# Kernel tuning notes

Hardware: AMD Instinct MI355X
Metric: run time of the kernel (lower is better)

Reference implementation:

```python
import jax, jax.numpy as jnp
import numpy as np

D_MODEL = 512
D_INNER = 1024   # expand * d_model
NH = 16          # heads (headdim 64)
HD = 64
NS = 16          # d_state
HID = 1024       # ff hidden = expand * d_model


def _ln(x, w, b, eps=1e-5):
    m = x.mean(-1, keepdims=True)
    v = ((x - m) ** 2).mean(-1, keepdims=True)
    return (x - m) * jax.lax.rsqrt(v + eps) * w + b


def _rms(x, w, eps=1e-5):
    return x * jax.lax.rsqrt((x * x).mean(-1, keepdims=True) + eps) * w


def _tree_scan(dt, xh, Bv, Cv, pidx, A):
    # dt:[B,T,W,H] xh:[B,T,W,H,P] Bv,Cv:[B,T,W,N] pidx:[B,T,W] A:[H]
    B_, T, W, H = dt.shape
    P = xh.shape[-1]
    N = Bv.shape[-1]
    h0 = jnp.zeros((B_, W, H, P, N), dt.dtype)
    xs = (jnp.moveaxis(dt, 1, 0), jnp.moveaxis(xh, 1, 0),
          jnp.moveaxis(Bv, 1, 0), jnp.moveaxis(Cv, 1, 0),
          jnp.moveaxis(pidx, 1, 0))

    def step(h, inp):
        dt_t, xh_t, b_t, c_t, p_t = inp
        # gather parent state from previous level along the width axis
        hp = jnp.take_along_axis(h, p_t[:, :, None, None, None], axis=1)  # [B,W,H,P,N]
        dA = jnp.exp(dt_t * A)                                            # [B,W,H]
        h_new = dA[..., None, None] * hp \
              + dt_t[..., None, None] * xh_t[..., None] * b_t[:, :, None, None, :]
        y_t = jnp.einsum('bwhpn,bwn->bwhp', h_new, c_t)
        return h_new, y_t

    _, ys = jax.lax.scan(step, h0, xs)
    return jnp.moveaxis(ys, 0, 1)  # [B,T,W,H,P]


def setup_inputs() -> dict:
    key = jax.random.key(0)
    ks = jax.random.split(key, 12)
    B, T, W = 8, 64, 16
    d_in_proj = 2 * D_INNER + 2 * NS + NH  # z | x | B | C | dt
    inp = {
        'x': jax.random.normal(ks[0], (B, T, W, D_MODEL), jnp.float32),
        'parent_pos': jax.random.randint(ks[1], (B, T, W), 0, W, dtype=jnp.int32),
        'ln1_w': jnp.ones((D_MODEL,), jnp.float32),
        'ln1_b': jnp.zeros((D_MODEL,), jnp.float32),
        'in_w': jax.random.normal(ks[2], (D_MODEL, d_in_proj), jnp.float32) * 0.02,
        'in_b': jnp.zeros((d_in_proj,), jnp.float32),
        'A_log': jnp.log(jax.random.uniform(ks[3], (NH,), jnp.float32, 1.0, 16.0)),
        'dt_bias': jnp.full((NH,), -4.0, jnp.float32),
        'Dp': jnp.ones((NH,), jnp.float32),
        'norm_w': jnp.ones((D_INNER,), jnp.float32),
        'out_w': jax.random.normal(ks[4], (D_INNER, D_MODEL), jnp.float32) * 0.02,
        'out_b': jnp.zeros((D_MODEL,), jnp.float32),
        'ln2_w': jnp.ones((D_MODEL,), jnp.float32),
        'ln2_b': jnp.zeros((D_MODEL,), jnp.float32),
        'ff1_w': jax.random.normal(ks[5], (D_MODEL, 2 * HID), jnp.float32) * 0.02,
        'ff1_b': jnp.zeros((2 * HID,), jnp.float32),
        'ff2_w': jax.random.normal(ks[6], (HID, D_MODEL), jnp.float32) * 0.02,
        'ff2_b': jnp.zeros((D_MODEL,), jnp.float32),
    }
    return inp


def reference(x, parent_pos, ln1_w, ln1_b, in_w, in_b, A_log, dt_bias, Dp,
              norm_w, out_w, out_b, ln2_w, ln2_b, ff1_w, ff1_b, ff2_w, ff2_b):
    # norm1 + TreeMamba2 + residual
    xn = _ln(x, ln1_w, ln1_b)
    proj = xn @ in_w + in_b
    z, xp, Bv, Cv, dtr = jnp.split(
        proj, [D_INNER, 2 * D_INNER, 2 * D_INNER + NS, 2 * D_INNER + 2 * NS], axis=-1)
    dt = jax.nn.softplus(dtr + dt_bias)            # [B,T,W,NH]
    A = -jnp.exp(A_log)                            # [NH]
    xh = xp.reshape(*xp.shape[:-1], NH, HD)        # [B,T,W,NH,HD]
    y = _tree_scan(dt, xh, Bv, Cv, parent_pos, A)  # [B,T,W,NH,HD]
    y = y + Dp[..., None] * xh                     # skip connection D*x
    y = y.reshape(*y.shape[:-2], D_INNER)
    y = _rms(y * jax.nn.silu(z), norm_w)           # gated RMSNorm
    y = y @ out_w + out_b
    x = y + x
    # norm2 + gated FF + residual
    yn = _ln(x, ln2_w, ln2_b)
    f = yn @ ff1_w + ff1_b
    f1, g = jnp.split(f, 2, axis=-1)
    f = (f1 * jax.nn.silu(g)) @ ff2_w + ff2_b
    return x + f
```

## Files before the change

### kernel.cpp

```cpp
#include <hip/hip_runtime.h>
#include <hip/hip_bf16.h>
#include <cmath>

#define D_MODEL 512
#define D_INNER 1024
#define NHEAD 16
#define HDIM 64
#define NSTATE 16
#define NB 8
#define NT 64
#define NW 16
#define MROWS 8192
#define NPROJ 2096

typedef __attribute__((ext_vector_type(8))) short short8;
typedef __attribute__((ext_vector_type(4))) float f32x4;
typedef __hip_bfloat16 bf16;
typedef unsigned int u32;
typedef unsigned short u16;

__device__ __forceinline__ u32 fbits(float f) { return __float_as_uint(f); }
__device__ __forceinline__ float ubits(u32 u) { return __uint_as_float(u); }
__device__ __forceinline__ u32 pack_bf(float a, float b) {
  return (fbits(b) & 0xffff0000u) | (fbits(a) >> 16);
}

template<int N> __device__ __forceinline__ void vmwait() {
  if constexpr (N == 0)      asm volatile("s_waitcnt vmcnt(0)" ::: "memory");
  else if constexpr (N == 2) asm volatile("s_waitcnt vmcnt(2)" ::: "memory");
  else if constexpr (N == 3) asm volatile("s_waitcnt vmcnt(3)" ::: "memory");
  else if constexpr (N == 4) asm volatile("s_waitcnt vmcnt(4)" ::: "memory");
  else if constexpr (N == 6) asm volatile("s_waitcnt vmcnt(6)" ::: "memory");
  else if constexpr (N == 8) asm volatile("s_waitcnt vmcnt(8)" ::: "memory");
  else static_assert(N == 0, "unsupported vmcnt");
}

__device__ __forceinline__ float block_sum(float v, float* sbuf) {
#pragma unroll
  for (int o = 32; o > 0; o >>= 1) v += __shfl_down(v, o, 64);
  int lane = threadIdx.x & 63, wid = threadIdx.x >> 6;
  if (lane == 0) sbuf[wid] = v;
  __syncthreads();
  if (threadIdx.x == 0) {
    float t = 0.f;
    for (int i = 0; i < 4; i++) t += sbuf[i];
    sbuf[0] = t;
  }
  __syncthreads();
  return sbuf[0];
}

__global__ __launch_bounds__(256) void ln512_bf16_kernel(
    const float* __restrict__ x, const float* __restrict__ w,
    const float* __restrict__ b, bf16* __restrict__ out) {
  __shared__ float s1[8], s2[8];
  int row = blockIdx.x;
  const float* xr = x + (size_t)row * D_MODEL;
  bf16* outr = out + (size_t)row * D_MODEL;
  int c0 = threadIdx.x, c1 = threadIdx.x + 256;
  float v0 = xr[c0], v1 = xr[c1];
  float s  = block_sum(v0 + v1, s1);
  float ss = block_sum(v0 * v0 + v1 * v1, s2);
  float mean = s * (1.f / 512.f);
  float var  = ss * (1.f / 512.f) - mean * mean;
  float inv  = rsqrtf(var + 1e-5f);
  outr[c0] = __float2bfloat16((v0 - mean) * inv * w[c0] + b[c0]);
  outr[c1] = __float2bfloat16((v1 - mean) * inv * w[c1] + b[c1]);
}

__global__ __launch_bounds__(256) void wconv_all_kernel(
    const float* __restrict__ in_w, bf16* __restrict__ in_wt,
    const float* __restrict__ out_w, bf16* __restrict__ out_wt,
    const float* __restrict__ ff1_w, bf16* __restrict__ ff1_wt,
    const float* __restrict__ ff2_w, bf16* __restrict__ ff2_wt) {
  __shared__ float tile[32][33];
  int id = blockIdx.x;
  const float* w; bf16* wt;
  int K, N, Npad, bx, by;
  if (id < 1088)      { w = in_w;  wt = in_wt;  K = 512;  N = NPROJ; Npad = 2176; bx = id % 68;  by = id / 68; }
  else if (id < 1600) { int j = id - 1088; w = out_w; wt = out_wt; K = 1024; N = 512;  Npad = 512;  bx = j % 16; by = j / 16; }
  else if (id < 2624) { int j = id - 1600; w = ff1_w; wt = ff1_wt; K = 512;  N = 2048; Npad = 2048; bx = j % 64; by = j / 64; }
  else                { int j = id - 2624; w = ff2_w; wt = ff2_wt; K = 1024; N = 512;  Npad = 512;  bx = j % 16; by = j / 16; }
  int n0 = bx * 32, k0 = by * 32;
  int tx = threadIdx.x & 31, ty = threadIdx.x >> 5;
#pragma unroll
  for (int i = 0; i < 4; i++) {
    int k = k0 + ty + i * 8, n = n0 + tx;
    tile[ty + i * 8][tx] = (k < K && n < N) ? w[(size_t)k * N + n] : 0.f;
  }
  __syncthreads();
#pragma unroll
  for (int i = 0; i < 4; i++) {
    int n = n0 + ty + i * 8, k = k0 + tx;
    if (n < Npad && k < K)
      wt[(size_t)n * K + k] = __float2bfloat16(tile[tx][ty + i * 8]);
  }
}

template<int BM, int BN, int WN, int MR, int NR>
__global__ __launch_bounds__(256) void mfma_gemm_kernel(
    const bf16* __restrict__ A, const bf16* __restrict__ Bt,
    const float* __restrict__ bias, int nbias,
    const float* __restrict__ resid,
    float* __restrict__ C, int ldc, int K) {
  constexpr int ROWS = BM + BN;
  constexpr int ISS  = ROWS / 64;
  __shared__ __align__(16) bf16 sAB[3][ROWS][32];

  int wid = threadIdx.x >> 6, lane = threadIdx.x & 63;
  int row0 = blockIdx.y * BM, col0 = blockIdx.x * BN;
  int wr = (wid / WN) * (MR * 16);
  int wc = (wid % WN) * (NR * 16);
  int lr = lane >> 2;
  int lc = (lane & 3) * 8;

  f32x4 acc[MR][NR];
#pragma unroll
  for (int m = 0; m < MR; m++)
#pragma unroll
    for (int n = 0; n < NR; n++) acc[m][n] = (f32x4){0.f, 0.f, 0.f, 0.f};

  auto stage = [&](int buf, int k0) {
#pragma unroll
    for (int i = 0; i < ISS; i++) {
      int rb = (wid * ISS + i) * 16;
      int r = rb + lr;
      const bf16* src = (r < BM)
          ? A  + (size_t)(row0 + r) * K + k0 + lc
          : Bt + (size_t)(col0 + (r - BM)) * K + k0 + lc;
      __builtin_amdgcn_global_load_lds(
          (const __attribute__((address_space(1))) void*)src,
          (__attribute__((address_space(3))) void*)&sAB[buf][rb][0], 16, 0, 0);
    }
  };

  stage(0, 0);
  stage(1, 32);
  int cur = 0;
  for (int k0 = 0; k0 < K; k0 += 32) {
    if (k0 + 32 < K) vmwait<ISS>(); else vmwait<0>();
    __builtin_amdgcn_s_barrier();
    asm volatile("" ::: "memory");
    if (k0 + 64 < K) stage(cur == 0 ? 2 : cur - 1, k0 + 64);
    short8 a[MR], b[NR];
    int kk = (lane >> 4) * 8;
#pragma unroll
    for (int m = 0; m < MR; m++)
      a[m] = *(const short8*)&sAB[cur][wr + m * 16 + (lane & 15)][kk];
#pragma unroll
    for (int n = 0; n < NR; n++)
      b[n] = *(const short8*)&sAB[cur][BM + wc + n * 16 + (lane & 15)][kk];
#pragma unroll
    for (int m = 0; m < MR; m++)
#pragma unroll
      for (int n = 0; n < NR; n++)
        acc[m][n] = __builtin_amdgcn_mfma_f32_16x16x32_bf16(a[m], b[n], acc[m][n], 0, 0, 0);
    asm volatile("" ::: "memory");
    cur = (cur == 2) ? 0 : cur + 1;
  }

  int crow = row0 + wr + (lane >> 4) * 4;
  int ccol = col0 + wc + (lane & 15);
#pragma unroll
  for (int m = 0; m < MR; m++) {
#pragma unroll
    for (int n = 0; n < NR; n++) {
      int colg = ccol + n * 16;
      float bv = bias ? ((colg < nbias) ? bias[colg] : 0.f) : 0.f;
#pragma unroll
      for (int j = 0; j < 4; j++) {
        int rowg = crow + m * 16 + j;
        float v = acc[m][n][j] + bv;
        if (resid) v += resid[(size_t)rowg * ldc + colg];
        C[(size_t)rowg * ldc + colg] = v;
      }
    }
  }
}

__global__ __launch_bounds__(256) void inproj_gemm_kernel(
    const bf16* __restrict__ A, const bf16* __restrict__ Bt,
    const float* __restrict__ bias,
    bf16* __restrict__ zb, bf16* __restrict__ xsc,
    float* __restrict__ aux, int K) {
  constexpr int BM = 128, ROWS = 256, ISS = 4;
  __shared__ __align__(16) bf16 sAB[3][ROWS][32];

  int wid = threadIdx.x >> 6, lane = threadIdx.x & 63;
  int row0 = blockIdx.y * BM, col0 = blockIdx.x * 128;
  int wr = (wid >> 1) * 64;
  int wc = (wid & 1) * 64;
  int lr = lane >> 2;
  int lc = (lane & 3) * 8;

  f32x4 acc[4][4];
#pragma unroll
  for (int m = 0; m < 4; m++)
#pragma unroll
    for (int n = 0; n < 4; n++) acc[m][n] = (f32x4){0.f, 0.f, 0.f, 0.f};

  auto stage = [&](int buf, int k0) {
#pragma unroll
    for (int i = 0; i < ISS; i++) {
      int rb = (wid * ISS + i) * 16;
      int r = rb + lr;
      const bf16* src = (r < BM)
          ? A  + (size_t)(row0 + r) * K + k0 + lc
          : Bt + (size_t)(col0 + (r - BM)) * K + k0 + lc;
      __builtin_amdgcn_global_load_lds(
          (const __attribute__((address_space(1))) void*)src,
          (__attribute__((address_space(3))) void*)&sAB[buf][rb][0], 16, 0, 0);
    }
  };

  stage(0, 0);
  stage(1, 32);
  int cur = 0;
  for (int k0 = 0; k0 < K; k0 += 32) {
    if (k0 + 32 < K) vmwait<ISS>(); else vmwait<0>();
    __builtin_amdgcn_s_barrier();
    asm volatile("" ::: "memory");
    if (k0 + 64 < K) stage(cur == 0 ? 2 : cur - 1, k0 + 64);
    short8 a[4], b[4];
    int kk = (lane >> 4) * 8;
#pragma unroll
    for (int m = 0; m < 4; m++)
      a[m] = *(const short8*)&sAB[cur][wr + m * 16 + (lane & 15)][kk];
#pragma unroll
    for (int n = 0; n < 4; n++)
      b[n] = *(const short8*)&sAB[cur][BM + wc + n * 16 + (lane & 15)][kk];
#pragma unroll
    for (int m = 0; m < 4; m++)
#pragma unroll
      for (int n = 0; n < 4; n++)
        acc[m][n] = __builtin_amdgcn_mfma_f32_16x16x32_bf16(a[m], b[n], acc[m][n], 0, 0, 0);
    asm volatile("" ::: "memory");
    cur = (cur == 2) ? 0 : cur + 1;
  }

  int crow = row0 + wr + (lane >> 4) * 4;
  int ccol = col0 + wc + (lane & 15);
#pragma unroll
  for (int m = 0; m < 4; m++) {
#pragma unroll
    for (int n = 0; n < 4; n++) {
      int colg = ccol + n * 16;
      float bv = (colg < NPROJ) ? bias[colg] : 0.f;
#pragma unroll
      for (int j = 0; j < 4; j++) {
        int rowg = crow + m * 16 + j;
        float v = acc[m][n][j] + bv;
        if (colg < 1024) {
          zb[(size_t)rowg * 1024 + colg] = __float2bfloat16(v);
        } else if (colg < 2048) {
          int cx = colg - 1024;
          int h = cx >> 6, p = cx & 63;
          int bb = rowg >> 10, t = (rowg >> 4) & 63, w = rowg & 15;
          size_t idx = ((((size_t)bb * 16 + h) * 4 + (p >> 4)) * 64 + t) * 256
                     + w * 16 + (p & 15);
          xsc[idx] = __float2bfloat16(v);
        } else if (colg < 2112) {
          aux[(size_t)rowg * 64 + (colg - 2048)] = v;
        }
      }
    }
  }
}

__global__ __launch_bounds__(256) void ff1_fused_kernel(
    const bf16* __restrict__ A, const bf16* __restrict__ Bt,
    const float* __restrict__ bias, bf16* __restrict__ out, int K) {
  constexpr int BM = 128, ROWS = 384, ISS = 6;
  __shared__ __align__(16) bf16 sAB[3][ROWS][32];

  int wid = threadIdx.x >> 6, lane = threadIdx.x & 63;
  int row0 = blockIdx.y * BM, col0 = blockIdx.x * 128;
  int wr = (wid >> 1) * 64;
  int wc = (wid & 1) * 64;
  int lr = lane >> 2;
  int lc = (lane & 3) * 8;

  f32x4 acc1[4][4], acc2[4][4];
#pragma unroll
  for (int m = 0; m < 4; m++)
#pragma unroll
    for (int n = 0; n < 4; n++) {
      acc1[m][n] = (f32x4){0.f, 0.f, 0.f, 0.f};
      acc2[m][n] = (f32x4){0.f, 0.f, 0.f, 0.f};
    }

  auto stage = [&](int buf, int k0) {
#pragma unroll
    for (int i = 0; i < ISS; i++) {
      int rb = (wid * ISS + i) * 16;
      int r = rb + lr;
      const bf16* src;
      if (r < BM)       src = A  + (size_t)(row0 + r) * K + k0 + lc;
      else if (r < 256) src = Bt + (size_t)(col0 + (r - 128)) * K + k0 + lc;
      else              src = Bt + (size_t)(1024 + col0 + (r - 256)) * K + k0 + lc;
      __builtin_amdgcn_global_load_lds(
          (const __attribute__((address_space(1))) void*)src,
          (__attribute__((address_space(3))) void*)&sAB[buf][rb][0], 16, 0, 0);
    }
  };

  stage(0, 0);
  stage(1, 32);
  int cur = 0;
  for (int k0 = 0; k0 < K; k0 += 32) {
    if (k0 + 32 < K) vmwait<ISS>(); else vmwait<0>();
    __builtin_amdgcn_s_barrier();
    asm volatile("" ::: "memory");
    if (k0 + 64 < K) stage(cur == 0 ? 2 : cur - 1, k0 + 64);
    short8 a[4], b1[4], b2[4];
    int kk = (lane >> 4) * 8;
#pragma unroll
    for (int m = 0; m < 4; m++)
      a[m] = *(const short8*)&sAB[cur][wr + m * 16 + (lane & 15)][kk];
#pragma unroll
    for (int n = 0; n < 4; n++) {
      b1[n] = *(const short8*)&sAB[cur][128 + wc + n * 16 + (lane & 15)][kk];
      b2[n] = *(const short8*)&sAB[cur][256 + wc + n * 16 + (lane & 15)][kk];
    }
#pragma unroll
    for (int m = 0; m < 4; m++)
#pragma unroll
      for (int n = 0; n < 4; n++) {
        acc1[m][n] = __builtin_amdgcn_mfma_f32_16x16x32_bf16(a[m], b1[n], acc1[m][n], 0, 0, 0);
        acc2[m][n] = __builtin_amdgcn_mfma_f32_16x16x32_bf16(a[m], b2[n], acc2[m][n], 0, 0, 0);
      }
    asm volatile("" ::: "memory");
    cur = (cur == 2) ? 0 : cur + 1;
  }

  int crow = row0 + wr + (lane >> 4) * 4;
  int ccol = col0 + wc + (lane & 15);
#pragma unroll
  for (int m = 0; m < 4; m++) {
#pragma unroll
    for (int n = 0; n < 4; n++) {
      int colg = ccol + n * 16;
      float bv1 = bias[colg];
      float bv2 = bias[1024 + colg];
#pragma unroll
      for (int j = 0; j < 4; j++) {
        int rowg = crow + m * 16 + j;
        float f1 = acc1[m][n][j] + bv1;
        float g  = acc2[m][n][j] + bv2;
        float sg = g / (1.f + expf(-g));
        out[(size_t)rowg * 1024 + colg] = __float2bfloat16(f1 * sg);
      }
    }
  }
}

__global__ __launch_bounds__(256) void tree_scan_kernel(
    const bf16* __restrict__ xsc, const float* __restrict__ aux,
    const int* __restrict__ parent,
    const float* __restrict__ A_log, const float* __restrict__ dt_bias,
    const float* __restrict__ Dp, bf16* __restrict__ y) {
  const int tid = threadIdx.x;
  const int ps = blockIdx.x & 3;
  const int h  = (blockIdx.x >> 2) & 15;
  const int b  = blockIdx.x >> 6;
  const int wid = tid >> 6;
  const int lane = tid & 63;
  const int w = lane >> 2;
  const int q = lane & 3;
  const int pl = wid * 4 + q;

  __shared__ __align__(16) u32   BCs[8][16][20];
  __shared__ __align__(16) float dAs[16][8];
  __shared__ __align__(16) float dtss[16][8];
  __shared__ __align__(16) int   pars[16][8];

  const float Ah  = -expf(A_log[h]);
  const float dtb = dt_bias[h];
  const float Dh  = Dp[h];
  const u16* xp = (const u16*)xsc
      + ((((size_t)b * 16 + h) * 4 + ps) * 64) * 256 + w * 16 + pl;
  const int ycol = (h << 6) + (ps << 4) + pl;

  float hst[16];
#pragma unroll
  for (int n = 0; n < 16; n++) hst[n] = 0.f;

  const int sp_t = tid >> 5, sp_w = (tid >> 1) & 15, sp_h = tid & 1;
  const int dt_t = tid >> 4, dt_w = tid & 15;

  u16 xpre[8];
  float4 bc0, bc1, bc2, bc3;
  float dtpre = 0.f;
  int papre = 0;

  auto issue = [&](int c) {
    const int t0 = c * 8;
#pragma unroll
    for (int tt = 0; tt < 8; tt++) xpre[tt] = xp[(size_t)(t0 + tt) * 256];
    size_t row = ((size_t)(b * NT + t0 + sp_t)) * NW + sp_w;
    const float* src = aux + row * 64 + sp_h * 16;
    bc0 = *(const float4*)&src[0];
    bc1 = *(const float4*)&src[4];
    bc2 = *(const float4*)&src[8];
    bc3 = *(const float4*)&src[12];
    if (tid < 128) {
      size_t r2 = ((size_t)(b * NT + t0 + dt_t)) * NW + dt_w;
      dtpre = aux[r2 * 64 + 32 + h];
      papre = parent[r2];
    }
  };

  issue(0);
  for (int c = 0; c < 8; c++) {
    const int t0 = c * 8;
    __syncthreads();
    float xv[8];
#pragma unroll
    for (int tt = 0; tt < 8; tt++) xv[tt] = ubits((u32)xpre[tt] << 16);
    if (tid < 128) {
      float dtr = dtpre + dtb;
      float dtv = (dtr > 20.f) ? dtr : log1pf(expf(dtr));
      dtss[dt_w][dt_t] = dtv;
      dAs[dt_w][dt_t]  = expf(dtv * Ah);
      pars[dt_w][dt_t] = papre;
    }
    {
      uint4 p0 = {pack_bf(bc0.x, bc0.y), pack_bf(bc0.z, bc0.w),
                  pack_bf(bc1.x, bc1.y), pack_bf(bc1.z, bc1.w)};
      uint4 p1 = {pack_bf(bc2.x, bc2.y), pack_bf(bc2.z, bc2.w),
                  pack_bf(bc3.x, bc3.y), pack_bf(bc3.z, bc3.w)};
      *(uint4*)&BCs[sp_t][sp_w][sp_h * 8]     = p0;
      *(uint4*)&BCs[sp_t][sp_w][sp_h * 8 + 4] = p1;
    }
    __syncthreads();
    float dAr[8], dtr8[8];
    int parr[8];
    *(float4*)&dAr[0]  = *(const float4*)&dAs[w][0];
    *(float4*)&dAr[4]  = *(const float4*)&dAs[w][4];
    *(float4*)&dtr8[0] = *(const float4*)&dtss[w][0];
    *(float4*)&dtr8[4] = *(const float4*)&dtss[w][4];
    *(int4*)&parr[0]   = *(const int4*)&pars[w][0];
    *(int4*)&parr[4]   = *(const int4*)&pars[w][4];
    if (c < 7) issue(c + 1);

#pragma unroll
    for (int tt = 0; tt < 8; tt++) {
      float dA  = dAr[tt];
      float dtx = dtr8[tt] * xv[tt];
      int   par = parr[tt];
      int gidx = (((par << 2) | q) << 2);
      u32 pk[8];
#pragma unroll
      for (int i = 0; i < 8; i++)
        pk[i] = (u32)__builtin_amdgcn_ds_bpermute(
            gidx, (int)pack_bf(hst[2 * i], hst[2 * i + 1]));
      uint4 bA = *(const uint4*)&BCs[tt][w][0];
      uint4 bB = *(const uint4*)&BCs[tt][w][4];
      uint4 cA = *(const uint4*)&BCs[tt][w][8];
      uint4 cB = *(const uint4*)&BCs[tt][w][12];
      u32 bwv[8] = {bA.x, bA.y, bA.z, bA.w, bB.x, bB.y, bB.z, bB.w};
      u32 cwv[8] = {cA.x, cA.y, cA.z, cA.w, cB.x, cB.y, cB.z, cB.w};
      float yv = 0.f;
#pragma unroll
      for (int i = 0; i < 8; i++) {
        u32 g = pk[i], bu = bwv[i], cu = cwv[i];
        float hp0 = ubits(g << 16);
        float hp1 = ubits(g & 0xffff0000u);
        float bl  = ubits(bu << 16), bh  = ubits(bu & 0xffff0000u);
        float cl  = ubits(cu << 16), ch  = ubits(cu & 0xffff0000u);
        float h0 = fmaf(dA, hp0, dtx * bl);
        float h1 = fmaf(dA, hp1, dtx * bh);
        hst[2 * i] = h0;
        hst[2 * i + 1] = h1;
        yv = fmaf(h0, cl, fmaf(h1, ch, yv));
      }
      size_t row = ((size_t)(b * NT + t0 + tt)) * NW + w;
      y[row * D_INNER + ycol] = __float2bfloat16(fmaf(Dh, xv[tt], yv));
    }
  }
}

__global__ __launch_bounds__(256) void gate_rms_kernel(
    const bf16* __restrict__ yin, const bf16* __restrict__ zb,
    const float* __restrict__ norm_w, bf16* __restrict__ out) {
  __shared__ float sbuf[8];
  int row = blockIdx.x;
  const bf16* yr = yin + (size_t)row * D_INNER;
  const bf16* zr = zb + (size_t)row * D_INNER;
  int c = threadIdx.x * 4;
  bf16 y4[4], z4[4];
  *(uint2*)y4 = *(const uint2*)&yr[c];
  *(uint2*)z4 = *(const uint2*)&zr[c];
  float gv[4];
  float ss = 0.f;
#pragma unroll
  for (int j = 0; j < 4; j++) {
    float z = __bfloat162float(z4[j]);
    float t = __bfloat162float(y4[j]) * (z / (1.f + expf(-z)));
    gv[j] = t;
    ss += t * t;
  }
  ss = block_sum(ss, sbuf);
  float scale = rsqrtf(ss * (1.f / 1024.f) + 1e-5f);
  bf16 o4[4];
#pragma unroll
  for (int j = 0; j < 4; j++) o4[j] = __float2bfloat16(gv[j] * scale * norm_w[c + j]);
  *(uint2*)&out[(size_t)row * D_INNER + c] = *(uint2*)o4;
}

extern "C" void kernel_launch(void* const* d_in, const int* in_sizes, int n_in,
                              void* d_out, int out_size, void* d_ws, size_t ws_size,
                              hipStream_t stream) {
  const float* x       = (const float*)d_in[0];
  const int*   parent  = (const int*)d_in[1];
  const float* ln1_w   = (const float*)d_in[2];
  const float* ln1_b   = (const float*)d_in[3];
  const float* in_w    = (const float*)d_in[4];
  const float* in_b    = (const float*)d_in[5];
  const float* A_log   = (const float*)d_in[6];
  const float* dt_bias = (const float*)d_in[7];
  const float* Dp      = (const float*)d_in[8];
  const float* norm_w  = (const float*)d_in[9];
  const float* out_w   = (const float*)d_in[10];
  const float* out_b   = (const float*)d_in[11];
  const float* ln2_w   = (const float*)d_in[12];
  const float* ln2_b   = (const float*)d_in[13];
  const float* ff1_w   = (const float*)d_in[14];
  const float* ff1_b   = (const float*)d_in[15];
  const float* ff2_w   = (const float*)d_in[16];
  const float* ff2_b   = (const float*)d_in[17];
  float* outp = (float*)d_out;

  char* wp = (char*)d_ws;
  bf16* xnb    = (bf16*)wp;  wp += (size_t)MROWS * D_MODEL * 2;
  bf16* in_wt  = (bf16*)wp;  wp += (size_t)2176 * D_MODEL * 2;
  bf16* out_wt = (bf16*)wp;  wp += (size_t)D_MODEL * D_INNER * 2;
  bf16* ff1_wt = (bf16*)wp;  wp += (size_t)2048 * D_MODEL * 2;
  bf16* ff2_wt = (bf16*)wp;  wp += (size_t)D_MODEL * D_INNER * 2;
  bf16* zb     = (bf16*)wp;  wp += (size_t)MROWS * D_INNER * 2;
  bf16* xsc    = (bf16*)wp;  wp += (size_t)MROWS * D_INNER * 2;
  float* aux   = (float*)wp; wp += (size_t)MROWS * 64 * 4;
  bf16* yb     = (bf16*)wp;  wp += (size_t)MROWS * D_INNER * 2;
  bf16* ygb    = (bf16*)wp;  wp += (size_t)MROWS * D_INNER * 2;
  float* xmid  = outp;

  dim3 blk(256);
  wconv_all_kernel<<<3136, blk, 0, stream>>>(
      in_w, in_wt, out_w, out_wt, ff1_w, ff1_wt, ff2_w, ff2_wt);
  ln512_bf16_kernel<<<MROWS, blk, 0, stream>>>(x, ln1_w, ln1_b, xnb);
  inproj_gemm_kernel<<<dim3(2176 / 128, MROWS / 128), blk, 0, stream>>>(
      xnb, in_wt, in_b, zb, xsc, aux, D_MODEL);
  tree_scan_kernel<<<NB * NHEAD * 4, blk, 0, stream>>>(xsc, aux, parent,
                                                       A_log, dt_bias, Dp, yb);
  gate_rms_kernel<<<MROWS, blk, 0, stream>>>(yb, zb, norm_w, ygb);
  mfma_gemm_kernel<64, 128, 4, 4, 2><<<dim3(D_MODEL / 128, MROWS / 64), blk, 0, stream>>>(
      ygb, out_wt, out_b, D_MODEL, x, xmid, D_MODEL, D_INNER);
  ln512_bf16_kernel<<<MROWS, blk, 0, stream>>>(xmid, ln2_w, ln2_b, xnb);
  ff1_fused_kernel<<<dim3(8, MROWS / 128), blk, 0, stream>>>(
      xnb, ff1_wt, ff1_b, yb, D_MODEL);
  mfma_gemm_kernel<64, 128, 4, 4, 2><<<dim3(D_MODEL / 128, MROWS / 64), blk, 0, stream>>>(
      yb, ff2_wt, ff2_b, D_MODEL, xmid, outp, D_MODEL, D_INNER);
}
```

Baseline: 204.9 us.

## Split tree-scan state dimension across lane pairs and double scan block count

The tree scan now gives each thread half of the 16 SSM states (8 instead of 16) and pairs lanes to cover one head-dim column, combining partial outputs with a lane xor-shuffle. The x layout written by the in-projection GEMM is changed to 8-column chunks, and the grid doubles to 1024 blocks. This targets the scan's long serial latency chain and low occupancy (only 512 blocks) by halving per-thread work and registers. The cost is an extra shuffle per step, half the lanes idle on the store, and duplicated B/C/dt staging across twice as many blocks.

Measured after the change: 210.1 us. 1.03x slower.

```diff
diff --git a/kernel.cpp b/kernel.cpp
--- a/kernel.cpp
+++ b/kernel.cpp
@@ -256,8 +256,8 @@
           int cx = colg - 1024;
           int h = cx >> 6, p = cx & 63;
           int bb = rowg >> 10, t = (rowg >> 4) & 63, w = rowg & 15;
-          size_t idx = ((((size_t)bb * 16 + h) * 4 + (p >> 4)) * 64 + t) * 256
-                     + w * 16 + (p & 15);
+          size_t idx = ((((size_t)bb * 16 + h) * 8 + (p >> 3)) * 64 + t) * 128
+                     + w * 8 + (p & 7);
           xsc[idx] = __float2bfloat16(v);
         } else if (colg < 2112) {
           aux[(size_t)rowg * 64 + (colg - 2048)] = v;
@@ -360,14 +360,15 @@
     const float* __restrict__ A_log, const float* __restrict__ dt_bias,
     const float* __restrict__ Dp, bf16* __restrict__ y) {
   const int tid = threadIdx.x;
-  const int ps = blockIdx.x & 3;
-  const int h  = (blockIdx.x >> 2) & 15;
-  const int b  = blockIdx.x >> 6;
-  const int wid = tid >> 6;
+  const int pc = blockIdx.x & 7;
+  const int h  = (blockIdx.x >> 3) & 15;
+  const int b  = blockIdx.x >> 7;
+  const int v = tid >> 6;
   const int lane = tid & 63;
   const int w = lane >> 2;
-  const int q = lane & 3;
-  const int pl = wid * 4 + q;
+  const int s = lane & 3;
+  const int nh = s & 1;
+  const int pl = v * 2 + (s >> 1);
 
   __shared__ __align__(16) u32   BCs[8][16][20];
   __shared__ __align__(16) float dAs[16][8];
@@ -378,12 +379,12 @@
   const float dtb = dt_bias[h];
   const float Dh  = Dp[h];
   const u16* xp = (const u16*)xsc
-      + ((((size_t)b * 16 + h) * 4 + ps) * 64) * 256 + w * 16 + pl;
-  const int ycol = (h << 6) + (ps << 4) + pl;
-
-  float hst[16];
-#pragma unroll
-  for (int n = 0; n < 16; n++) hst[n] = 0.f;
+      + ((((size_t)b * 16 + h) * 8 + pc) * 64) * 128 + w * 8 + pl;
+  const int ycol = (h << 6) + pc * 8 + pl;
+
+  float hst[8];
+#pragma unroll
+  for (int n = 0; n < 8; n++) hst[n] = 0.f;
 
   const int sp_t = tid >> 5, sp_w = (tid >> 1) & 15, sp_h = tid & 1;
   const int dt_t = tid >> 4, dt_w = tid & 15;
@@ -396,7 +397,7 @@
   auto issue = [&](int c) {
     const int t0 = c * 8;
 #pragma unroll
-    for (int tt = 0; tt < 8; tt++) xpre[tt] = xp[(size_t)(t0 + tt) * 256];
+    for (int tt = 0; tt < 8; tt++) xpre[tt] = xp[(size_t)(t0 + tt) * 128];
     size_t row = ((size_t)(b * NT + t0 + sp_t)) * NW + sp_w;
     const float* src = aux + row * 64 + sp_h * 16;
     bc0 = *(const float4*)&src[0];
@@ -429,8 +430,8 @@
                   pack_bf(bc1.x, bc1.y), pack_bf(bc1.z, bc1.w)};
       uint4 p1 = {pack_bf(bc2.x, bc2.y), pack_bf(bc2.z, bc2.w),
                   pack_bf(bc3.x, bc3.y), pack_bf(bc3.z, bc3.w)};
-      *(uint4*)&BCs[sp_t][sp_w][sp_h * 8]     = p0;
-      *(uint4*)&BCs[sp_t][sp_w][sp_h * 8 + 4] = p1;
+      *(uint4*)&BCs[sp_t][sp_w][sp_h * 4]      = p0;
+      *(uint4*)&BCs[sp_t][sp_w][10 + sp_h * 4] = p1;
     }
     __syncthreads();
     float dAr[8], dtr8[8];
@@ -448,21 +449,19 @@
       float dA  = dAr[tt];
       float dtx = dtr8[tt] * xv[tt];
       int   par = parr[tt];
-      int gidx = (((par << 2) | q) << 2);
-      u32 pk[8];
-#pragma unroll
-      for (int i = 0; i < 8; i++)
+      int gidx = (((par << 2) | s) << 2);
+      u32 pk[4];
+#pragma unroll
+      for (int i = 0; i < 4; i++)
         pk[i] = (u32)__builtin_amdgcn_ds_bpermute(
             gidx, (int)pack_bf(hst[2 * i], hst[2 * i + 1]));
-      uint4 bA = *(const uint4*)&BCs[tt][w][0];
-      uint4 bB = *(const uint4*)&BCs[tt][w][4];
-      uint4 cA = *(const uint4*)&BCs[tt][w][8];
-      uint4 cB = *(const uint4*)&BCs[tt][w][12];
-      u32 bwv[8] = {bA.x, bA.y, bA.z, bA.w, bB.x, bB.y, bB.z, bB.w};
-      u32 cwv[8] = {cA.x, cA.y, cA.z, cA.w, cB.x, cB.y, cB.z, cB.w};
+      uint4 bu4 = *(const uint4*)&BCs[tt][w][nh * 10];
+      uint4 cu4 = *(const uint4*)&BCs[tt][w][nh * 10 + 4];
+      u32 bwv[4] = {bu4.x, bu4.y, bu4.z, bu4.w};
+      u32 cwv[4] = {cu4.x, cu4.y, cu4.z, cu4.w};
       float yv = 0.f;
 #pragma unroll
-      for (int i = 0; i < 8; i++) {
+      for (int i = 0; i < 4; i++) {
         u32 g = pk[i], bu = bwv[i], cu = cwv[i];
         float hp0 = ubits(g << 16);
         float hp1 = ubits(g & 0xffff0000u);
@@ -474,8 +473,11 @@
         hst[2 * i + 1] = h1;
         yv = fmaf(h0, cl, fmaf(h1, ch, yv));
       }
-      size_t row = ((size_t)(b * NT + t0 + tt)) * NW + w;
-      y[row * D_INNER + ycol] = __float2bfloat16(fmaf(Dh, xv[tt], yv));
+      float yv_tot = yv + __shfl_xor(yv, 1, 64);
+      if (nh == 0) {
+        size_t row = ((size_t)(b * NT + t0 + tt)) * NW + w;
+        y[row * D_INNER + ycol] = __float2bfloat16(fmaf(Dh, xv[tt], yv_tot));
+      }
     }
   }
 }
@@ -550,7 +552,7 @@
   ln512_bf16_kernel<<<MROWS, blk, 0, stream>>>(x, ln1_w, ln1_b, xnb);
   inproj_gemm_kernel<<<dim3(2176 / 128, MROWS / 128), blk, 0, stream>>>(
       xnb, in_wt, in_b, zb, xsc, aux, D_MODEL);
-  tree_scan_kernel<<<NB * NHEAD * 4, blk, 0, stream>>>(xsc, aux, parent,
+  tree_scan_kernel<<<NB * NHEAD * 8, blk, 0, stream>>>(xsc, aux, parent,
                                                        A_log, dt_bias, Dp, yb);
   gate_rms_kernel<<<MROWS, blk, 0, stream>>>(yb, zb, norm_w, ygb);
   mfma_gemm_kernel<64, 128, 4, 4, 2><<<dim3(D_MODEL / 128, MROWS / 64), blk, 0, stream>>>(
```

## Fuse gated RMSNorm into out-projection GEMM and fold norm weight into weights

Applied to the files above, without the earlier changes.

Removes the separate gate_rms kernel and its intermediate bf16 buffer. The out-projection GEMM now loads y and z, applies the SiLU gate on the fly, accumulates per-row sum of squares during the K loop, and scales the accumulator by the row rsqrt in the epilogue. norm_w is folded into the transposed out_w during weight conversion. This saves one global round trip and a launch. In exchange, each of the 4 column blocks recomputes the gate for the same rows, and the A operand loads go through registers instead of direct-to-LDS.

After: 216.2 us. 5.5% more time.

```diff
diff --git a/kernel.cpp b/kernel.cpp
--- a/kernel.cpp
+++ b/kernel.cpp
@@ -71,14 +71,15 @@
 __global__ __launch_bounds__(256) void wconv_all_kernel(
     const float* __restrict__ in_w, bf16* __restrict__ in_wt,
     const float* __restrict__ out_w, bf16* __restrict__ out_wt,
+    const float* __restrict__ norm_w,
     const float* __restrict__ ff1_w, bf16* __restrict__ ff1_wt,
     const float* __restrict__ ff2_w, bf16* __restrict__ ff2_wt) {
   __shared__ float tile[32][33];
   int id = blockIdx.x;
-  const float* w; bf16* wt;
+  const float* w; bf16* wt; const float* sc = nullptr;
   int K, N, Npad, bx, by;
   if (id < 1088)      { w = in_w;  wt = in_wt;  K = 512;  N = NPROJ; Npad = 2176; bx = id % 68;  by = id / 68; }
-  else if (id < 1600) { int j = id - 1088; w = out_w; wt = out_wt; K = 1024; N = 512;  Npad = 512;  bx = j % 16; by = j / 16; }
+  else if (id < 1600) { int j = id - 1088; w = out_w; wt = out_wt; sc = norm_w; K = 1024; N = 512;  Npad = 512;  bx = j % 16; by = j / 16; }
   else if (id < 2624) { int j = id - 1600; w = ff1_w; wt = ff1_wt; K = 512;  N = 2048; Npad = 2048; bx = j % 64; by = j / 64; }
   else                { int j = id - 2624; w = ff2_w; wt = ff2_wt; K = 1024; N = 512;  Npad = 512;  bx = j % 16; by = j / 16; }
   int n0 = bx * 32, k0 = by * 32;
@@ -89,11 +90,12 @@
     tile[ty + i * 8][tx] = (k < K && n < N) ? w[(size_t)k * N + n] : 0.f;
   }
   __syncthreads();
+  float s = sc ? sc[k0 + tx] : 1.f;
 #pragma unroll
   for (int i = 0; i < 4; i++) {
     int n = n0 + ty + i * 8, k = k0 + tx;
     if (n < Npad && k < K)
-      wt[(size_t)n * K + k] = __float2bfloat16(tile[tx][ty + i * 8]);
+      wt[(size_t)n * K + k] = __float2bfloat16(tile[tx][ty + i * 8] * s);
   }
 }
 
@@ -354,6 +356,110 @@
   }
 }
 
+__global__ __launch_bounds__(256) void outproj_fused_kernel(
+    const bf16* __restrict__ yb, const bf16* __restrict__ zb,
+    const bf16* __restrict__ Wt, const float* __restrict__ out_b,
+    const float* __restrict__ x, float* __restrict__ xmid) {
+  constexpr int BM = 64, BN = 128, K = 1024;
+  __shared__ __align__(16) bf16 sA[2][BM][32];
+  __shared__ __align__(16) bf16 sB[2][BN][32];
+  __shared__ float srow[BM];
+
+  const int tid = threadIdx.x;
+  const int wid = tid >> 6, lane = tid & 63;
+  const int row0 = blockIdx.y * BM, col0 = blockIdx.x * BN;
+  const int wc = wid * 32;
+  const int lr = lane >> 2, lc = (lane & 3) * 8;
+  const int ar = tid >> 2, akc = (tid & 3) * 8;
+
+  f32x4 acc[4][2];
+#pragma unroll
+  for (int m = 0; m < 4; m++)
+#pragma unroll
+    for (int n = 0; n < 2; n++) acc[m][n] = (f32x4){0.f, 0.f, 0.f, 0.f};
+  float ssp = 0.f;
+
+  uint4 yv, zv;
+  auto stageB = [&](int buf, int k0) {
+#pragma unroll
+    for (int i = 0; i < 2; i++) {
+      int rb = (wid * 2 + i) * 16;
+      const bf16* src = Wt + (size_t)(col0 + rb + lr) * K + k0 + lc;
+      __builtin_amdgcn_global_load_lds(
+          (const __attribute__((address_space(1))) void*)src,
+          (__attribute__((address_space(3))) void*)&sB[buf][rb][0], 16, 0, 0);
+    }
+  };
+  auto loadA = [&](int k0) {
+    yv = *(const uint4*)&yb[(size_t)(row0 + ar) * D_INNER + k0 + akc];
+    zv = *(const uint4*)&zb[(size_t)(row0 + ar) * D_INNER + k0 + akc];
+  };
+  auto writeA = [&](int buf) {
+    bf16 ya[8], za[8], tb[8];
+    *(uint4*)ya = yv;
+    *(uint4*)za = zv;
+#pragma unroll
+    for (int j = 0; j < 8; j++) {
+      float z = __bfloat162float(za[j]);
+      float t = __bfloat162float(ya[j]) * (z / (1.f + expf(-z)));
+      ssp += t * t;
+      tb[j] = __float2bfloat16(t);
+    }
+    *(uint4*)&sA[buf][ar][akc] = *(uint4*)tb;
+  };
+
+  stageB(0, 0);
+  loadA(0);
+  vmwait<0>();
+  writeA(0);
+  __syncthreads();
+
+  int cur = 0;
+  for (int k0 = 0; k0 < K; k0 += 32) {
+    bool more = k0 + 32 < K;
+    if (more) { stageB(cur ^ 1, k0 + 32); loadA(k0 + 32); }
+    short8 a[4], b[2];
+    int kk = (lane >> 4) * 8;
+#pragma unroll
+    for (int m = 0; m < 4; m++)
+      a[m] = *(const short8*)&sA[cur][m * 16 + (lane & 15)][kk];
+#pragma unroll
+    for (int n = 0; n < 2; n++)
+      b[n] = *(const short8*)&sB[cur][wc + n * 16 + (lane & 15)][kk];
+#pragma unroll
+    for (int m = 0; m < 4; m++)
+#pragma unroll
+      for (int n = 0; n < 2; n++)
+        acc[m][n] = __builtin_amdgcn_mfma_f32_16x16x32_bf16(a[m], b[n], acc[m][n], 0, 0, 0);
+    if (more) { vmwait<0>(); writeA(cur ^ 1); }
+    __syncthreads();
+    cur ^= 1;
+  }
+
+  ssp += __shfl_xor(ssp, 1, 4);
+  ssp += __shfl_xor(ssp, 2, 4);
+  if ((tid & 3) == 0) srow[ar] = rsqrtf(ssp * (1.f / 1024.f) + 1e-5f);
+  __syncthreads();
+
+  int ccol = col0 + wc + (lane & 15);
+#pragma unroll
+  for (int m = 0; m < 4; m++) {
+#pragma unroll
+    for (int j = 0; j < 4; j++) {
+      int rl = (lane >> 4) * 4 + m * 16 + j;
+      int rowg = row0 + rl;
+      float sr = srow[rl];
+#pragma unroll
+      for (int n = 0; n < 2; n++) {
+        int colg = ccol + n * 16;
+        float v = acc[m][n][j] * sr + out_b[colg]
+                + x[(size_t)rowg * D_MODEL + colg];
+        xmid[(size_t)rowg * D_MODEL + colg] = v;
+      }
+    }
+  }
+}
+
 __global__ __launch_bounds__(256) void tree_scan_kernel(
     const bf16* __restrict__ xsc, const float* __restrict__ aux,
     const int* __restrict__ parent,
@@ -478,34 +584,6 @@
       y[row * D_INNER + ycol] = __float2bfloat16(fmaf(Dh, xv[tt], yv));
     }
   }
-}
-
-__global__ __launch_bounds__(256) void gate_rms_kernel(
-    const bf16* __restrict__ yin, const bf16* __restrict__ zb,
-    const float* __restrict__ norm_w, bf16* __restrict__ out) {
-  __shared__ float sbuf[8];
-  int row = blockIdx.x;
-  const bf16* yr = yin + (size_t)row * D_INNER;
-  const bf16* zr = zb + (size_t)row * D_INNER;
-  int c = threadIdx.x * 4;
-  bf16 y4[4], z4[4];
-  *(uint2*)y4 = *(const uint2*)&yr[c];
-  *(uint2*)z4 = *(const uint2*)&zr[c];
-  float gv[4];
-  float ss = 0.f;
-#pragma unroll
-  for (int j = 0; j < 4; j++) {
-    float z = __bfloat162float(z4[j]);
-    float t = __bfloat162float(y4[j]) * (z / (1.f + expf(-z)));
-    gv[j] = t;
-    ss += t * t;
-  }
-  ss = block_sum(ss, sbuf);
-  float scale = rsqrtf(ss * (1.f / 1024.f) + 1e-5f);
-  bf16 o4[4];
-#pragma unroll
-  for (int j = 0; j < 4; j++) o4[j] = __float2bfloat16(gv[j] * scale * norm_w[c + j]);
-  *(uint2*)&out[(size_t)row * D_INNER + c] = *(uint2*)o4;
 }
 
 extern "C" void kernel_launch(void* const* d_in, const int* in_sizes, int n_in,
@@ -541,20 +619,18 @@
   bf16* xsc    = (bf16*)wp;  wp += (size_t)MROWS * D_INNER * 2;
   float* aux   = (float*)wp; wp += (size_t)MROWS * 64 * 4;
   bf16* yb     = (bf16*)wp;  wp += (size_t)MROWS * D_INNER * 2;
-  bf16* ygb    = (bf16*)wp;  wp += (size_t)MROWS * D_INNER * 2;
   float* xmid  = outp;
 
   dim3 blk(256);
   wconv_all_kernel<<<3136, blk, 0, stream>>>(
-      in_w, in_wt, out_w, out_wt, ff1_w, ff1_wt, ff2_w, ff2_wt);
+      in_w, in_wt, out_w, out_wt, norm_w, ff1_w, ff1_wt, ff2_w, ff2_wt);
   ln512_bf16_kernel<<<MROWS, blk, 0, stream>>>(x, ln1_w, ln1_b, xnb);
   inproj_gemm_kernel<<<dim3(2176 / 128, MROWS / 128), blk, 0, stream>>>(
       xnb, in_wt, in_b, zb, xsc, aux, D_MODEL);
   tree_scan_kernel<<<NB * NHEAD * 4, blk, 0, stream>>>(xsc, aux, parent,
                                                        A_log, dt_bias, Dp, yb);
-  gate_rms_kernel<<<MROWS, blk, 0, stream>>>(yb, zb, norm_w, ygb);
-  mfma_gemm_kernel<64, 128, 4, 4, 2><<<dim3(D_MODEL / 128, MROWS / 64), blk, 0, stream>>>(
-      ygb, out_wt, out_b, D_MODEL, x, xmid, D_MODEL, D_INNER);
+  outproj_fused_kernel<<<dim3(D_MODEL / 128, MROWS / 64), blk, 0, stream>>>(
+      yb, zb, out_wt, out_b, x, xmid);
   ln512_bf16_kernel<<<MROWS, blk, 0, stream>>>(xmid, ln2_w, ln2_b, xnb);
   ff1_fused_kernel<<<dim3(8, MROWS / 128), blk, 0, stream>>>(
       xnb, ff1_wt, ff1_b, yb, D_MODEL);
```
